# Optimization experiments

Hardware: AMD Instinct MI355X
Metric: run time of the kernel (lower is better)

The kernel has to match this reference:

```python
import jax, jax.numpy as jnp
import numpy as np

NUM_ROUTERS = 8
K = 2
IN_DIM = 384
HID = 64
TEMP = 1.0
AUX_COEF = 0.05
EPS = 1e-12


def _l2norm(v, axis=-1):
    n = jnp.sqrt(jnp.sum(v * v, axis=axis, keepdims=True))
    return v / jnp.maximum(n, EPS)


def setup_inputs() -> dict:
    key = jax.random.key(0)
    ks = jax.random.split(key, 10)
    B, E = 8192, 1024
    s = 1.0 / np.sqrt(IN_DIM)
    return {
        "x": jax.random.normal(ks[0], (B, IN_DIM), jnp.float32),
        "reasoning_embeddings": jax.random.normal(ks[1], (E, IN_DIM), jnp.float32),
        "random_num": jax.random.uniform(ks[2], (B, 1), jnp.float32),
        "gate_w": jax.random.normal(ks[3], (IN_DIM, NUM_ROUTERS), jnp.float32) * s,
        "gate_b": jnp.zeros((NUM_ROUTERS,), jnp.float32),
        "Uw": jax.random.normal(ks[4], (NUM_ROUTERS, IN_DIM, HID), jnp.float32) * s,
        "Ub": jnp.zeros((NUM_ROUTERS, HID), jnp.float32),
        "Vw": jax.random.normal(ks[5], (NUM_ROUTERS, IN_DIM, HID), jnp.float32) * s,
        "Vb": jnp.zeros((NUM_ROUTERS, HID), jnp.float32),
    }


def reference(x, reasoning_embeddings, random_num, gate_w, gate_b, Uw, Ub, Vw, Vb):
    B = x.shape[0]
    # gate
    logits = x @ gate_w + gate_b                              # [B, R]
    probs = jax.nn.softmax(logits, axis=-1)
    topk_vals, topk_idxs = jax.lax.top_k(logits, K)           # [B, K]
    topk_mask = jax.nn.one_hot(topk_idxs, NUM_ROUTERS).sum(axis=1)  # [B, R]
    aux_loss = NUM_ROUTERS * (probs.mean(0) * topk_mask.mean(0)).sum() * AUX_COEF

    # all routers, batched (replaces the per-(i,j) python loop)
    xu = _l2norm(jnp.einsum("bd,rdh->rbh", x, Uw) + Ub[:, None, :])          # [R, B, H]
    ev = _l2norm(jnp.einsum("ed,rdh->reh", reasoning_embeddings, Vw) + Vb[:, None, :])  # [R, E, H]
    scores = jnp.einsum("rbh,reh->rbe", xu, ev)               # [R, B, E]
    all_out = jax.nn.softmax(scores / TEMP, axis=-1)          # [R, B, E]

    # gather top-k experts per sample
    all_out_b = jnp.transpose(all_out, (1, 0, 2))             # [B, R, E]
    router_outputs = jnp.take_along_axis(all_out_b, topk_idxs[:, :, None], axis=1)  # [B, K, E]

    gate_weights = jax.nn.softmax(topk_vals, axis=-1)[:, :, None]  # [B, K, 1]
    rea_probs = jnp.sum(router_outputs * gate_weights, axis=1)     # [B, E]

    # categorical sampling via inverse-CDF
    scores_cumsum = jnp.cumsum(rea_probs, axis=1)
    selected_index = jnp.argmax((scores_cumsum > random_num).astype(jnp.float32), axis=1)  # [B]
    log_probs = jnp.log(rea_probs[jnp.arange(B), selected_index])[:, None]  # [B, 1]
    return selected_index, log_probs, aux_loss
```

## Files before the change

kernel.cpp:

```cpp
#include <hip/hip_runtime.h>
#include <math.h>

#define B 8192
#define E 1024
#define D 384
#define H 64
#define R 8
#define NCHUNK 16
#define CHUNK_E 64
#define NPOS 16448

#define WS_COUNTS   0u
#define WS_CURSORS  32u
#define WS_PS       64u
#define WS_TOP2     256u
#define WS_GW       65792u
#define WS_POSMAP   131328u
#define WS_LIST     196864u
#define WS_EVN      262656u
#define WS_XUN      2359808u
#define WS_C        6570496u

__global__ __launch_bounds__(256) void k_gate(
    const float* __restrict__ x, const float* __restrict__ gate_w,
    const float* __restrict__ gate_b, int2* __restrict__ top2,
    float2* __restrict__ gwv, int* __restrict__ counts, float* __restrict__ ps)
{
  __shared__ __align__(16) float gwT[R * 388];
  __shared__ float psl[R];
  __shared__ int   cl[R];
  int tid = threadIdx.x;
  for (int idx = tid; idx < D * R; idx += 256) {
    int k = idx >> 3, r = idx & 7;
    gwT[r * 388 + k] = gate_w[idx];
  }
  if (tid < R) { psl[tid] = 0.f; cl[tid] = 0; }
  __syncthreads();

  int l = tid & 63;
  int r = tid & 7;
  int b = blockIdx.x * 32 + (tid >> 3);
  float acc = gate_b[r];
  const float4* x4 = (const float4*)(x + (size_t)b * D);
  const float*  gr = gwT + r * 388;
#pragma unroll 4
  for (int q = 0; q < 96; ++q) {
    float4 xv = x4[q];
    float4 gv = *(const float4*)&gr[q * 4];
    acc = fmaf(xv.x, gv.x, acc);
    acc = fmaf(xv.y, gv.y, acc);
    acc = fmaf(xv.z, gv.z, acc);
    acc = fmaf(xv.w, gv.w, acc);
  }
  float lv[R];
#pragma unroll
  for (int rr = 0; rr < R; ++rr) lv[rr] = __shfl(acc, (l & ~7) + rr);
  int i0 = 0; float v0 = lv[0];
#pragma unroll
  for (int rr = 1; rr < R; ++rr) if (lv[rr] > v0) { v0 = lv[rr]; i0 = rr; }
  int i1 = (i0 == 0) ? 1 : 0; float v1 = lv[i1];
#pragma unroll
  for (int rr = 0; rr < R; ++rr)
    if (rr != i0 && lv[rr] > v1) { v1 = lv[rr]; i1 = rr; }
  float se = 0.f;
#pragma unroll
  for (int rr = 0; rr < R; ++rr) se += expf(lv[rr] - v0);
  float p = expf(acc - v0) / se;
  if (r == 0) {
    float e10 = expf(v1 - v0);
    top2[b] = make_int2(i0, i1);
    gwv[b]  = make_float2(1.f / (1.f + e10), e10 / (1.f + e10));
  }
  float pa = p;
  int   ca = (r == i0 ? 1 : 0) + (r == i1 ? 1 : 0);
#pragma unroll
  for (int m = 8; m < 64; m <<= 1) {
    pa += __shfl_xor(pa, m);
    ca += __shfl_xor(ca, m);
  }
  if (l < 8) { atomicAdd(&psl[r], pa); atomicAdd(&cl[r], ca); }
  __syncthreads();
  if (tid < R) { atomicAdd(&ps[tid], psl[tid]); atomicAdd(&counts[tid], cl[tid]); }
}

__global__ __launch_bounds__(256) void k_scatter(
    const int2* __restrict__ top2, const int* __restrict__ counts,
    const float* __restrict__ ps, int* __restrict__ cursors,
    int* __restrict__ list, int2* __restrict__ posmap, float* __restrict__ out_aux)
{
  __shared__ int lc[R];
  __shared__ int lbase[R];
  __shared__ int offs[R];
  int tid = threadIdx.x;
  if (tid < R) lc[tid] = 0;
  __syncthreads();
  if (tid == 0) {
    int o = 0;
    for (int r2 = 0; r2 < R; ++r2) { offs[r2] = o; o += (min(counts[r2], B) + 7) & ~7; }
  }
  __syncthreads();
  int b = min(blockIdx.x * 256 + tid, B - 1);
  int2 t = top2[b];
  t.x &= 7; t.y &= 7;
  int p0 = atomicAdd(&lc[t.x], 1);
  int p1 = atomicAdd(&lc[t.y], 1);
  __syncthreads();
  if (tid < R) lbase[tid] = atomicAdd(&cursors[tid], lc[tid]);
  __syncthreads();
  int i0 = min(offs[t.x] + lbase[t.x] + p0, NPOS - 1);
  int i1 = min(offs[t.y] + lbase[t.y] + p1, NPOS - 1);
  list[i0] = b * 2 + 0;
  list[i1] = b * 2 + 1;
  posmap[b] = make_int2(i0, i1);
  if (blockIdx.x == 0 && tid == 0) {
    float s = 0.f;
    for (int r2 = 0; r2 < R; ++r2)
      s += (ps[r2] / (float)B) * ((float)min(counts[r2], B) / (float)B);
    out_aux[0] = (float)R * s * 0.05f;
  }
}

__global__ __launch_bounds__(256) void k_proj(
    const float* __restrict__ re, const float* __restrict__ x,
    const float* __restrict__ Vw, const float* __restrict__ Vb,
    const float* __restrict__ Uw, const float* __restrict__ Ub,
    const int* __restrict__ list, const int* __restrict__ counts,
    float* __restrict__ evnT, float* __restrict__ xunP)
{
  int tid = threadIdx.x;
  int lane = tid & 63;
  int wv = tid >> 6;
  int bid = blockIdx.x;

  bool isE = (bid < 256);
  int r, g, n = 32, base = 0;
  const float *W, *bias;
  if (isE) {
    r = bid >> 5; g = bid & 31;
    W = Vw + (size_t)r * (D * H); bias = Vb + r * H;
  } else {
    int idx = bid - 256;
    r = idx >> 8; g = idx & 255;
    int cnt = min(counts[r], B);
    if (g * 32 >= cnt) return;
    n = min(32, cnt - g * 32);
    for (int rr = 0; rr < r; ++rr) base += (min(counts[rr], B) + 7) & ~7;
    base += g * 32;
    W = Uw + (size_t)r * (D * H); bias = Ub + r * H;
  }
  int row0 = wv * 8;
  if (row0 >= n) return;

  const float* arow[8];
#pragma unroll
  for (int i = 0; i < 8; ++i) {
    int rr = min(row0 + i, n - 1);
    if (isE) {
      arow[i] = re + (size_t)(g * 32 + rr) * D;
    } else {
      int gl = list[min(base + rr, NPOS - 1)];
      gl = min(max(gl, 0), 2 * B - 1);
      arow[i] = x + (size_t)(gl >> 1) * D;
    }
  }
  float bv = bias[lane];
  float acc[8];
#pragma unroll
  for (int i = 0; i < 8; ++i) acc[i] = bv;

  for (int c = 0; c < 6; ++c) {
    float w[64];
#pragma unroll
    for (int k = 0; k < 64; ++k) w[k] = W[(size_t)(c * 64 + k) * H + lane];
    float xa[8];
#pragma unroll
    for (int i = 0; i < 8; ++i) xa[i] = arow[i][c * 64 + lane];
#pragma unroll
    for (int k = 0; k < 64; ++k) {
      float wk = w[k];
#pragma unroll
      for (int i = 0; i < 8; ++i) {
        float s = __uint_as_float(__builtin_amdgcn_readlane(__float_as_uint(xa[i]), k));
        acc[i] = fmaf(s, wk, acc[i]);
      }
    }
  }

  float rn[8];
#pragma unroll
  for (int i = 0; i < 8; ++i) {
    float ss = acc[i] * acc[i];
#pragma unroll
    for (int m = 1; m < 64; m <<= 1) ss += __shfl_xor(ss, m);
    rn[i] = 1.f / fmaxf(sqrtf(ss), 1e-12f);
  }

  if (isE) {
    int e0 = g * 32 + row0;
    float4 o0, o1;
    o0.x = acc[0] * rn[0]; o0.y = acc[1] * rn[1];
    o0.z = acc[2] * rn[2]; o0.w = acc[3] * rn[3];
    o1.x = acc[4] * rn[4]; o1.y = acc[5] * rn[5];
    o1.z = acc[6] * rn[6]; o1.w = acc[7] * rn[7];
    float* dst = evnT + (size_t)(r * 64 + lane) * 1024 + e0;
    *(float4*)dst = o0;
    *(float4*)(dst + 4) = o1;
  } else {
#pragma unroll
    for (int i = 0; i < 8; ++i)
      if (row0 + i < n)
        xunP[(size_t)(base + row0 + i) * H + lane] = acc[i] * rn[i];
  }
}

__global__ __launch_bounds__(256) void k_pass1(
    const float* __restrict__ evnT, const float* __restrict__ xunP,
    const int* __restrict__ counts, float* __restrict__ C)
{
  __shared__ __align__(16) float Xt[64 * 128];
  __shared__ __align__(16) float Et[64 * 128];
  __shared__ int cntL[R];
  int tid = threadIdx.x;
  if (tid < R) cntL[tid] = min(counts[tid], B);
  __syncthreads();

  int bid = blockIdx.x;
  int et    = bid & 7;
  int stile = (bid >> 3) & 63;
  int r     = bid >> 9;
  int cnt = cntL[r];
  if (cnt <= 0 || stile * 128 >= cnt) return;
  int off = 0;
  for (int rr = 0; rr < r; ++rr) off += (cntL[rr] + 7) & ~7;
  off += stile * 128;
  int n = min(128, cnt - stile * 128);
  int ebase = et * 128;

  {
    int row = tid >> 1;
    int rc  = min(row, n - 1);
    const float4* src = (const float4*)(xunP + (size_t)(off + rc) * H);
    int hq0 = (tid & 1) * 8;
#pragma unroll
    for (int q = 0; q < 8; ++q) {
      float4 v = src[hq0 + q];
      int h = (hq0 + q) * 4;
      Xt[(h + 0) * 128 + row] = v.x;
      Xt[(h + 1) * 128 + row] = v.y;
      Xt[(h + 2) * 128 + row] = v.z;
      Xt[(h + 3) * 128 + row] = v.w;
    }
  }
  {
#pragma unroll
    for (int q = 0; q < 8; ++q) {
      int idx = tid + 256 * q;
      int h = idx >> 5, e4 = idx & 31;
      float4 v = *(const float4*)(evnT + (size_t)(r * 64 + h) * 1024 + ebase + e4 * 4);
      *(float4*)&Et[h * 128 + e4 * 4] = v;
    }
  }
  __syncthreads();

  int sg = tid >> 4, egr = tid & 15;
  float acc[8][8];
#pragma unroll
  for (int i = 0; i < 8; ++i)
#pragma unroll
    for (int j = 0; j < 8; ++j) acc[i][j] = 0.f;

#pragma unroll 4
  for (int k = 0; k < 64; ++k) {
    float4 xa = *(const float4*)&Xt[k * 128 + sg * 8];
    float4 xb = *(const float4*)&Xt[k * 128 + sg * 8 + 4];
    float4 ea = *(const float4*)&Et[k * 128 + egr * 4];
    float4 eb = *(const float4*)&Et[k * 128 + 64 + egr * 4];
    const float* pa = (const float*)&xa;
    const float* pb = (const float*)&xb;
    const float* qa = (const float*)&ea;
    const float* qb = (const float*)&eb;
#pragma unroll
    for (int i = 0; i < 4; ++i)
#pragma unroll
      for (int j = 0; j < 4; ++j) {
        acc[i][j]         = fmaf(pa[i], qa[j], acc[i][j]);
        acc[i][j + 4]     = fmaf(pa[i], qb[j], acc[i][j + 4]);
        acc[i + 4][j]     = fmaf(pb[i], qa[j], acc[i + 4][j]);
        acc[i + 4][j + 4] = fmaf(pb[i], qb[j], acc[i + 4][j + 4]);
      }
  }

#pragma unroll
  for (int i = 0; i < 8; ++i) {
    float cA = expf(acc[i][0]) + expf(acc[i][1]) + expf(acc[i][2]) + expf(acc[i][3]);
    float cB = expf(acc[i][4]) + expf(acc[i][5]) + expf(acc[i][6]) + expf(acc[i][7]);
#pragma unroll
    for (int m = 1; m < 16; m <<= 1) {
      cA += __shfl_xor(cA, m);
      cB += __shfl_xor(cB, m);
    }
    int s = sg * 8 + i;
    if (egr == 0 && s < n) {
      C[(size_t)(off + s) * NCHUNK + et * 2]     = cA;
      C[(size_t)(off + s) * NCHUNK + et * 2 + 1] = cB;
    }
  }
}

__global__ __launch_bounds__(256) void k_pass2(
    const float* __restrict__ evnT, const float* __restrict__ xunP,
    const float* __restrict__ C, const int2* __restrict__ top2,
    const int2* __restrict__ posmap, const float2* __restrict__ gwv,
    const float* __restrict__ rnd, float* __restrict__ out)
{
  int tid = threadIdx.x;
  int lane = tid & 63;
  int b = blockIdx.x * 4 + (tid >> 6);
  if (b >= B) return;
  int2 t2 = top2[b];
  t2.x &= 7; t2.y &= 7;
  int2 pm = posmap[b];
  pm.x = min(max(pm.x, 0), NPOS - 1);
  pm.y = min(max(pm.y, 0), NPOS - 1);
  float2 gw = gwv[b];
  float rv = rnd[b];

  const float4* C04 = (const float4*)(C + (size_t)pm.x * NCHUNK);
  const float4* C14 = (const float4*)(C + (size_t)pm.y * NCHUNK);
  float c0[NCHUNK], c1[NCHUNK];
#pragma unroll
  for (int q = 0; q < 4; ++q) {
    float4 v0 = C04[q], v1 = C14[q];
    c0[q*4+0]=v0.x; c0[q*4+1]=v0.y; c0[q*4+2]=v0.z; c0[q*4+3]=v0.w;
    c1[q*4+0]=v1.x; c1[q*4+1]=v1.y; c1[q*4+2]=v1.z; c1[q*4+3]=v1.w;
  }
  float S0 = 0.f, S1 = 0.f;
#pragma unroll
  for (int j = 0; j < NCHUNK; ++j) { S0 += c0[j]; S1 += c1[j]; }
  float a0 = gw.x / S0, a1 = gw.y / S1;
  int cstar = -1; float prefix = 0.f; float run = 0.f;
#pragma unroll
  for (int j = 0; j < NCHUNK; ++j) {
    float nrun = run + (c0[j] * a0 + c1[j] * a1);
    if (cstar < 0 && nrun > rv) { cstar = j; prefix = run; }
    run = nrun;
  }
  float rtgt = rv;
  if (cstar < 0) { cstar = 0; prefix = 0.f; rtgt = -1.0f; }

  float xu0 = xunP[(size_t)pm.x * H + lane];
  float xu1 = xunP[(size_t)pm.y * H + lane];
  const float* E0 = evnT + (size_t)t2.x * 64 * 1024 + cstar * CHUNK_E + lane;
  const float* E1 = evnT + (size_t)t2.y * 64 * 1024 + cstar * CHUNK_E + lane;
  float d0 = 0.f, d1 = 0.f;
#pragma unroll 16
  for (int h = 0; h < 64; ++h) {
    float w0 = __shfl(xu0, h);
    float w1 = __shfl(xu1, h);
    d0 = fmaf(E0[(size_t)h * 1024], w0, d0);
    d1 = fmaf(E1[(size_t)h * 1024], w1, d1);
  }
  float rea = expf(d0) * a0 + expf(d1) * a1;
  float sc = rea;
#pragma unroll
  for (int d = 1; d < 64; d <<= 1) {
    float o = __shfl_up(sc, d);
    if (lane >= d) sc += o;
  }
  float cum = prefix + sc;
  unsigned long long m2 = __ballot(cum > rtgt);
  int estar = (m2 == 0ull) ? 63 : (int)__builtin_ctzll(m2);
  float p = __shfl(rea, estar);
  if (lane == 0) {
    int sel = cstar * CHUNK_E + estar;
    out[b]     = (float)sel;
    out[B + b] = logf(p);
  }
}

extern "C" void kernel_launch(void* const* d_in, const int* in_sizes, int n_in,
                              void* d_out, int out_size, void* d_ws, size_t ws_size,
                              hipStream_t stream)
{
  (void)in_sizes; (void)n_in; (void)out_size; (void)ws_size;
  const float* x      = (const float*)d_in[0];
  const float* re     = (const float*)d_in[1];
  const float* rnd    = (const float*)d_in[2];
  const float* gate_w = (const float*)d_in[3];
  const float* gate_b = (const float*)d_in[4];
  const float* Uw     = (const float*)d_in[5];
  const float* Ub     = (const float*)d_in[6];
  const float* Vw     = (const float*)d_in[7];
  const float* Vb     = (const float*)d_in[8];
  char* ws = (char*)d_ws;
  int*    counts  = (int*)(ws + WS_COUNTS);
  int*    cursors = (int*)(ws + WS_CURSORS);
  float*  ps      = (float*)(ws + WS_PS);
  int2*   top2    = (int2*)(ws + WS_TOP2);
  float2* gwv     = (float2*)(ws + WS_GW);
  int2*   posmap  = (int2*)(ws + WS_POSMAP);
  int*    list    = (int*)(ws + WS_LIST);
  float*  evnT    = (float*)(ws + WS_EVN);
  float*  xunP    = (float*)(ws + WS_XUN);
  float*  Cc      = (float*)(ws + WS_C);
  float* out = (float*)d_out;

  hipMemsetAsync(ws, 0, 256, stream);
  k_gate   <<<256,  256, 0, stream>>>(x, gate_w, gate_b, top2, gwv, counts, ps);
  k_scatter<<<32,   256, 0, stream>>>(top2, counts, ps, cursors, list, posmap, out + 2 * B);
  k_proj   <<<2304, 256, 0, stream>>>(re, x, Vw, Vb, Uw, Ub, list, counts, evnT, xunP);
  k_pass1  <<<4096, 256, 0, stream>>>(evnT, xunP, counts, Cc);
  k_pass2  <<<2048, 256, 0, stream>>>(evnT, xunP, Cc, top2, posmap, gwv, rnd, out);
}
```

Before: 212.7 us.

## Replace readlane projection with shared-memory tiled split-K GEMM plus finalize kernel

The per-wave readlane projection kernel becomes a 64x64 LDS-tiled GEMM that splits K in two, followed by a separate kernel that sums the two partials, adds bias and L2-normalizes. Router segments are padded to multiples of 64 so each tile maps to a single router. The pass1 E tile gets a padded stride to avoid LDS bank conflicts. In exchange the change adds a kernel launch and extra global traffic for the partial buffers, and the normalize kernel writes evnT with strided scalar stores.

```diff
diff --git a/kernel.cpp b/kernel.cpp
--- a/kernel.cpp
+++ b/kernel.cpp
@@ -8,7 +8,8 @@
 #define R 8
 #define NCHUNK 16
 #define CHUNK_E 64
-#define NPOS 16448
+#define NPOS 16896
+#define NROW 25088
 
 #define WS_COUNTS   0u
 #define WS_CURSORS  32u
@@ -17,9 +18,11 @@
 #define WS_GW       65792u
 #define WS_POSMAP   131328u
 #define WS_LIST     196864u
-#define WS_EVN      262656u
-#define WS_XUN      2359808u
-#define WS_C        6570496u
+#define WS_EVN      264448u
+#define WS_XUN      2361600u
+#define WS_C        6686976u
+#define WS_BUFA     7768320u
+#define WS_BUFB     14190848u
 
 __global__ __launch_bounds__(256) void k_gate(
     const float* __restrict__ x, const float* __restrict__ gate_w,
@@ -96,7 +99,7 @@
   __syncthreads();
   if (tid == 0) {
     int o = 0;
-    for (int r2 = 0; r2 < R; ++r2) { offs[r2] = o; o += (min(counts[r2], B) + 7) & ~7; }
+    for (int r2 = 0; r2 < R; ++r2) { offs[r2] = o; o += (min(counts[r2], B) + 63) & ~63; }
   }
   __syncthreads();
   int b = min(blockIdx.x * 256 + tid, B - 1);
@@ -120,96 +123,123 @@
   }
 }
 
-__global__ __launch_bounds__(256) void k_proj(
+__global__ __launch_bounds__(256) void k_projgemm(
     const float* __restrict__ re, const float* __restrict__ x,
-    const float* __restrict__ Vw, const float* __restrict__ Vb,
-    const float* __restrict__ Uw, const float* __restrict__ Ub,
+    const float* __restrict__ Vw, const float* __restrict__ Uw,
     const int* __restrict__ list, const int* __restrict__ counts,
-    float* __restrict__ evnT, float* __restrict__ xunP)
+    float* __restrict__ bufA, float* __restrict__ bufB)
+{
+  __shared__ __align__(16) float At[64 * 64];
+  __shared__ __align__(16) float Wt[64 * 64];
+  int tid = threadIdx.x;
+  int bid = blockIdx.x;
+  int tile = bid >> 1, ks = bid & 1;
+  int row0 = tile * 64;
+
+  const float* Wsrc;
+  if (row0 < 8192) {
+    Wsrc = Vw + (size_t)(row0 >> 10) * (D * H);
+  } else {
+    int pos0 = row0 - 8192;
+    int r = 0, baseq = 0;
+    for (int rr = 0; rr < R; ++rr) {
+      if (pos0 >= baseq) r = rr;
+      baseq += (min(counts[rr], B) + 63) & ~63;
+    }
+    Wsrc = Uw + (size_t)r * (D * H);
+  }
+
+  int srow = tid & 63, sq = tid >> 6;
+  const float* arow;
+  if (row0 < 8192) {
+    arow = re + (size_t)((row0 + srow) & 1023) * D;
+  } else {
+    int pos = row0 - 8192 + srow;
+    int gl = list[min(pos, NPOS - 1)];
+    gl = min(max(gl, 0), 2 * B - 1);
+    arow = x + (size_t)(gl >> 1) * D;
+  }
+  int wk = tid >> 2, wc = tid & 3;
+  int rg = tid >> 4, hg = tid & 15;
+
+  float acc[4][4];
+#pragma unroll
+  for (int i = 0; i < 4; ++i)
+#pragma unroll
+    for (int j = 0; j < 4; ++j) acc[i][j] = 0.f;
+
+  for (int kt = 0; kt < 3; ++kt) {
+    int kb = ks * 192 + kt * 64;
+    __syncthreads();
+#pragma unroll
+    for (int q = 0; q < 4; ++q) {
+      float4 v = *(const float4*)&arow[kb + sq * 16 + q * 4];
+      int k0 = sq * 16 + q * 4;
+      At[(k0 + 0) * 64 + srow] = v.x;
+      At[(k0 + 1) * 64 + srow] = v.y;
+      At[(k0 + 2) * 64 + srow] = v.z;
+      At[(k0 + 3) * 64 + srow] = v.w;
+    }
+    const float* wrow = Wsrc + (size_t)(kb + wk) * H;
+#pragma unroll
+    for (int q = 0; q < 4; ++q) {
+      float4 v = *(const float4*)&wrow[(wc * 4 + q) * 4];
+      *(float4*)&Wt[wk * 64 + (wc * 4 + q) * 4] = v;
+    }
+    __syncthreads();
+#pragma unroll 8
+    for (int k = 0; k < 64; ++k) {
+      float4 a4 = *(const float4*)&At[k * 64 + rg * 4];
+      float4 w4 = *(const float4*)&Wt[k * 64 + hg * 4];
+      const float* ap = (const float*)&a4;
+      const float* wp = (const float*)&w4;
+#pragma unroll
+      for (int i = 0; i < 4; ++i)
+#pragma unroll
+        for (int j = 0; j < 4; ++j) acc[i][j] = fmaf(ap[i], wp[j], acc[i][j]);
+    }
+  }
+  float* dst = (ks ? bufB : bufA) + (size_t)row0 * H;
+#pragma unroll
+  for (int i = 0; i < 4; ++i) {
+    float4 o;
+    o.x = acc[i][0]; o.y = acc[i][1]; o.z = acc[i][2]; o.w = acc[i][3];
+    *(float4*)&dst[(rg * 4 + i) * H + hg * 4] = o;
+  }
+}
+
+__global__ __launch_bounds__(256) void k_projfin(
+    const float* __restrict__ bufA, const float* __restrict__ bufB,
+    const float* __restrict__ Vb, const float* __restrict__ Ub,
+    const int* __restrict__ counts, float* __restrict__ evnT,
+    float* __restrict__ xunP)
 {
   int tid = threadIdx.x;
   int lane = tid & 63;
-  int wv = tid >> 6;
-  int bid = blockIdx.x;
-
-  bool isE = (bid < 256);
-  int r, g, n = 32, base = 0;
-  const float *W, *bias;
+  int row0 = blockIdx.x * 32 + (tid >> 6) * 8;
+  bool isE = row0 < 8192;
+  int r = 0;
   if (isE) {
-    r = bid >> 5; g = bid & 31;
-    W = Vw + (size_t)r * (D * H); bias = Vb + r * H;
+    r = row0 >> 10;
   } else {
-    int idx = bid - 256;
-    r = idx >> 8; g = idx & 255;
-    int cnt = min(counts[r], B);
-    if (g * 32 >= cnt) return;
-    n = min(32, cnt - g * 32);
-    for (int rr = 0; rr < r; ++rr) base += (min(counts[rr], B) + 7) & ~7;
-    base += g * 32;
-    W = Uw + (size_t)r * (D * H); bias = Ub + r * H;
-  }
-  int row0 = wv * 8;
-  if (row0 >= n) return;
-
-  const float* arow[8];
+    int pos0 = row0 - 8192;
+    int baseq = 0;
+    for (int rr = 0; rr < R; ++rr) {
+      if (pos0 >= baseq) r = rr;
+      baseq += (min(counts[rr], B) + 63) & ~63;
+    }
+  }
+  float bias = isE ? Vb[r * H + lane] : Ub[r * H + lane];
 #pragma unroll
   for (int i = 0; i < 8; ++i) {
-    int rr = min(row0 + i, n - 1);
-    if (isE) {
-      arow[i] = re + (size_t)(g * 32 + rr) * D;
-    } else {
-      int gl = list[min(base + rr, NPOS - 1)];
-      gl = min(max(gl, 0), 2 * B - 1);
-      arow[i] = x + (size_t)(gl >> 1) * D;
-    }
-  }
-  float bv = bias[lane];
-  float acc[8];
-#pragma unroll
-  for (int i = 0; i < 8; ++i) acc[i] = bv;
-
-  for (int c = 0; c < 6; ++c) {
-    float w[64];
-#pragma unroll
-    for (int k = 0; k < 64; ++k) w[k] = W[(size_t)(c * 64 + k) * H + lane];
-    float xa[8];
-#pragma unroll
-    for (int i = 0; i < 8; ++i) xa[i] = arow[i][c * 64 + lane];
-#pragma unroll
-    for (int k = 0; k < 64; ++k) {
-      float wk = w[k];
-#pragma unroll
-      for (int i = 0; i < 8; ++i) {
-        float s = __uint_as_float(__builtin_amdgcn_readlane(__float_as_uint(xa[i]), k));
-        acc[i] = fmaf(s, wk, acc[i]);
-      }
-    }
-  }
-
-  float rn[8];
-#pragma unroll
-  for (int i = 0; i < 8; ++i) {
-    float ss = acc[i] * acc[i];
+    int row = row0 + i;
+    float s = bufA[(size_t)row * H + lane] + bufB[(size_t)row * H + lane] + bias;
+    float ss = s * s;
 #pragma unroll
     for (int m = 1; m < 64; m <<= 1) ss += __shfl_xor(ss, m);
-    rn[i] = 1.f / fmaxf(sqrtf(ss), 1e-12f);
-  }
-
-  if (isE) {
-    int e0 = g * 32 + row0;
-    float4 o0, o1;
-    o0.x = acc[0] * rn[0]; o0.y = acc[1] * rn[1];
-    o0.z = acc[2] * rn[2]; o0.w = acc[3] * rn[3];
-    o1.x = acc[4] * rn[4]; o1.y = acc[5] * rn[5];
-    o1.z = acc[6] * rn[6]; o1.w = acc[7] * rn[7];
-    float* dst = evnT + (size_t)(r * 64 + lane) * 1024 + e0;
-    *(float4*)dst = o0;
-    *(float4*)(dst + 4) = o1;
-  } else {
-#pragma unroll
-    for (int i = 0; i < 8; ++i)
-      if (row0 + i < n)
-        xunP[(size_t)(base + row0 + i) * H + lane] = acc[i] * rn[i];
+    float v = s / fmaxf(sqrtf(ss), 1e-12f);
+    if (isE) evnT[(size_t)(r * 64 + lane) * 1024 + (row & 1023)] = v;
+    else     xunP[(size_t)(row - 8192) * H + lane] = v;
   }
 }
 
@@ -218,7 +248,7 @@
     const int* __restrict__ counts, float* __restrict__ C)
 {
   __shared__ __align__(16) float Xt[64 * 128];
-  __shared__ __align__(16) float Et[64 * 128];
+  __shared__ __align__(16) float Et[64 * 132];
   __shared__ int cntL[R];
   int tid = threadIdx.x;
   if (tid < R) cntL[tid] = min(counts[tid], B);
@@ -231,7 +261,7 @@
   int cnt = cntL[r];
   if (cnt <= 0 || stile * 128 >= cnt) return;
   int off = 0;
-  for (int rr = 0; rr < r; ++rr) off += (cntL[rr] + 7) & ~7;
+  for (int rr = 0; rr < r; ++rr) off += (cntL[rr] + 63) & ~63;
   off += stile * 128;
   int n = min(128, cnt - stile * 128);
   int ebase = et * 128;
@@ -257,7 +287,7 @@
       int idx = tid + 256 * q;
       int h = idx >> 5, e4 = idx & 31;
       float4 v = *(const float4*)(evnT + (size_t)(r * 64 + h) * 1024 + ebase + e4 * 4);
-      *(float4*)&Et[h * 128 + e4 * 4] = v;
+      *(float4*)&Et[h * 132 + e4 * 4] = v;
     }
   }
   __syncthreads();
@@ -273,8 +303,8 @@
   for (int k = 0; k < 64; ++k) {
     float4 xa = *(const float4*)&Xt[k * 128 + sg * 8];
     float4 xb = *(const float4*)&Xt[k * 128 + sg * 8 + 4];
-    float4 ea = *(const float4*)&Et[k * 128 + egr * 4];
-    float4 eb = *(const float4*)&Et[k * 128 + 64 + egr * 4];
+    float4 ea = *(const float4*)&Et[k * 132 + egr * 4];
+    float4 eb = *(const float4*)&Et[k * 132 + 64 + egr * 4];
     const float* pa = (const float*)&xa;
     const float* pb = (const float*)&xb;
     const float* qa = (const float*)&ea;
@@ -403,12 +433,15 @@
   float*  evnT    = (float*)(ws + WS_EVN);
   float*  xunP    = (float*)(ws + WS_XUN);
   float*  Cc      = (float*)(ws + WS_C);
+  float*  bufA    = (float*)(ws + WS_BUFA);
+  float*  bufB    = (float*)(ws + WS_BUFB);
   float* out = (float*)d_out;
 
   hipMemsetAsync(ws, 0, 256, stream);
-  k_gate   <<<256,  256, 0, stream>>>(x, gate_w, gate_b, top2, gwv, counts, ps);
-  k_scatter<<<32,   256, 0, stream>>>(top2, counts, ps, cursors, list, posmap, out + 2 * B);
-  k_proj   <<<2304, 256, 0, stream>>>(re, x, Vw, Vb, Uw, Ub, list, counts, evnT, xunP);
-  k_pass1  <<<4096, 256, 0, stream>>>(evnT, xunP, counts, Cc);
-  k_pass2  <<<2048, 256, 0, stream>>>(evnT, xunP, Cc, top2, posmap, gwv, rnd, out);
-}
+  k_gate    <<<256,  256, 0, stream>>>(x, gate_w, gate_b, top2, gwv, counts, ps);
+  k_scatter <<<32,   256, 0, stream>>>(top2, counts, ps, cursors, list, posmap, out + 2 * B);
+  k_projgemm<<<784,  256, 0, stream>>>(re, x, Vw, Uw, list, counts, bufA, bufB);
+  k_projfin <<<784,  256, 0, stream>>>(bufA, bufB, Vb, Ub, counts, evnT, xunP);
+  k_pass1   <<<4096, 256, 0, stream>>>(evnT, xunP, counts, Cc);
+  k_pass2   <<<2048, 256, 0, stream>>>(evnT, xunP, Cc, top2, posmap, gwv, rnd, out);
+}
```

Result: faster. 180.7 us (-15.0%).
